# Optimization experiments

Measured on AMD Instinct MI355X. Metric: run time of the kernel, lower is better.

The kernel has to match this reference:

```python
import jax, jax.numpy as jnp
import numpy as np

N0 = 3190      # len(x_0), hardcoded via `edges[0] += 3190` in the source
N_NEW = 16384  # test batch size
T = 60         # num_features (seq len)
C = 5          # n_diagnosis_codes
H = 20         # emb_size == hidden_size == input_size
HC = 15        # hidden_channels
NCLS = 3
L = 4          # lstm layers
K = 5          # neighbors kept per new node
E0 = 31900     # edges in pickled base graph


def setup_inputs() -> dict:
    key = jax.random.key(0)
    ks = jax.random.split(key, 21)
    s = 0.2  # ~ pytorch uniform(-1/sqrt(20), 1/sqrt(20)) scale, avoids LSTM saturation
    return {
        "x": jax.random.uniform(ks[0], (T, N_NEW, C), jnp.float32),
        "x_0": jax.random.normal(ks[1], (N0, H), jnp.float32),
        "emb_w": jax.random.normal(ks[2], (C, H), jnp.float32) * s,
        "lstm_Wih": jax.random.normal(ks[3], (L, 4 * H, H), jnp.float32) * s,
        "lstm_Whh": jax.random.normal(ks[4], (L, 4 * H, H), jnp.float32) * s,
        "lstm_bih": jax.random.normal(ks[5], (L, 4 * H), jnp.float32) * s,
        "lstm_bhh": jax.random.normal(ks[6], (L, 4 * H), jnp.float32) * s,
        "attn_w1": jax.random.normal(ks[7], (64, H), jnp.float32) * s,
        "attn_b1": jax.random.normal(ks[8], (64,), jnp.float32) * s,
        "attn_w2": jax.random.normal(ks[9], (1, 64), jnp.float32) * s,
        "attn_b2": jax.random.normal(ks[10], (1,), jnp.float32) * s,
        "w1l": jax.random.normal(ks[11], (HC, H), jnp.float32) * s,
        "w1r": jax.random.normal(ks[12], (HC, H), jnp.float32) * s,
        "b1": jax.random.normal(ks[13], (HC,), jnp.float32) * s,
        "w2l": jax.random.normal(ks[14], (H, HC), jnp.float32) * s,
        "w2r": jax.random.normal(ks[15], (H, HC), jnp.float32) * s,
        "b2": jax.random.normal(ks[16], (H,), jnp.float32) * s,
        "wlin": jax.random.normal(ks[17], (NCLS, H), jnp.float32) * s,
        "blin": jax.random.normal(ks[18], (NCLS,), jnp.float32) * s,
        "edge_0": jax.random.randint(ks[19], (2, E0), 0, N0, dtype=jnp.int32),
    }


def _lstm_layer(inp, Wih, Whh, bih, bhh):
    # inp: [T, B, D]; PyTorch gate order i, f, g, o
    B = inp.shape[1]
    Hh = Whh.shape[1]
    b = bih + bhh

    def step(carry, xt):
        h, c = carry
        g = xt @ Wih.T + h @ Whh.T + b  # [B, 4H]
        i, f, gg, o = jnp.split(g, 4, axis=-1)
        c = jax.nn.sigmoid(f) * c + jax.nn.sigmoid(i) * jnp.tanh(gg)
        h = jax.nn.sigmoid(o) * jnp.tanh(c)
        return (h, c), h

    init = (jnp.zeros((B, Hh), inp.dtype), jnp.zeros((B, Hh), inp.dtype))
    _, hs = jax.lax.scan(step, init, inp)
    return hs  # [T, B, H]


def _sage(xn, src, dst, Wl, Wr, b, num_nodes):
    # PyG SAGEConv (mean aggr): lin_l(mean_{j in N(i)} x_j) + lin_r(x_i); bias in lin_l
    msg = xn[src]  # gather  [E, D]
    s = jax.ops.segment_sum(msg, dst, num_segments=num_nodes)
    cnt = jax.ops.segment_sum(jnp.ones(dst.shape, xn.dtype), dst, num_segments=num_nodes)
    mean = s / jnp.maximum(cnt, 1.0)[:, None]
    return mean @ Wl.T + xn @ Wr.T + b


def _forward(x, x_0, emb_w, lstm_Wih, lstm_Whh, lstm_bih, lstm_bhh,
             attn_w1, attn_b1, attn_w2, attn_b2,
             w1l, w1r, b1, w2l, w2r, b2, wlin, blin, edge_0):
    # (x[...,None] * emb_w).sum over codes == weighted embedding mix, then relu
    h = jax.nn.relu(jnp.einsum('tnc,ce->tne', x, emb_w))  # [T, N_new, H]
    for l in range(L):
        h = _lstm_layer(h, lstm_Wih[l], lstm_Whh[l], lstm_bih[l], lstm_bhh[l])
    enc = jnp.transpose(h, (1, 0, 2))  # [N_new, T, H]
    # SelfAttention: Linear(H,64) -> ReLU -> Linear(64,1) -> softmax over time
    hid = jax.nn.relu(jnp.einsum('nth,kh->ntk', enc, attn_w1) + attn_b1)
    energy = jnp.einsum('ntk,ok->nto', hid, attn_w2) + attn_b2  # [N_new, T, 1]
    w = jax.nn.softmax(energy[..., 0], axis=1)
    xh = jnp.sum(enc * w[..., None], axis=1)  # [N_new, H]
    # cosine similarity against the fixed base nodes (memory-bound [N_new, N0] matrix)
    a = (xh @ x_0.T) / jnp.linalg.norm(xh, axis=1, keepdims=True) / jnp.linalg.norm(x_0, axis=1)[None, :]
    top6_v, top6_i = jax.lax.top_k(a, 6)
    # per-row branch: drop self-match (sim == 1.0) else drop 6th neighbor
    exact = top6_v[:, 0] == 1.0
    top5 = jnp.where(exact[:, None], top6_i[:, 1:], top6_i[:, :K])  # [N_new, 5]
    # torch.where(A>0) enumerates row-major with sorted cols; rows have exactly 5 ones
    src = jnp.sort(top5, axis=1).reshape(-1)  # base-node endpoints
    dst = jnp.repeat(jnp.arange(N_NEW, dtype=src.dtype), K) + N0  # new-node endpoints (offset)
    edges_new = jnp.stack([src, dst])  # direction base -> new (after the swap in source)
    edges_all = jnp.concatenate([edge_0.astype(src.dtype), edges_new], axis=1)
    xcat = jnp.concatenate([x_0, xh], axis=0)  # [N0 + N_new, H]
    num_nodes = N0 + N_NEW
    o = jax.nn.relu(_sage(xcat, edge_0[0], edge_0[1], w1l, w1r, b1, num_nodes))
    # F.dropout with training=False is identity (test-time module)
    o = _sage(o, edges_all[0], edges_all[1], w2l, w2r, b2, num_nodes)
    o = jax.nn.softmax(o @ wlin.T + blin, axis=1)
    return o[N0:]


def reference(x, x_0, emb_w, lstm_Wih, lstm_Whh, lstm_bih, lstm_bhh,
              attn_w1, attn_b1, attn_w2, attn_b2,
              w1l, w1r, b1, w2l, w2r, b2, wlin, blin, edge_0):
    return _forward(x, x_0, emb_w, lstm_Wih, lstm_Whh, lstm_bih, lstm_bhh,
                    attn_w1, attn_b1, attn_w2, attn_b2,
                    w1l, w1r, b1, w2l, w2r, b2, wlin, blin, edge_0)
```

## Files before the change

kernel.cpp:

```cpp
#include <hip/hip_runtime.h>
#include <math.h>

#define T_ 60
#define N_ 16384
#define C_ 5
#define H_ 20
#define G_ 80
#define HC_ 15
#define N0_ 3190
#define E0_ 31900
#define K_ 5

#define OFF_SEQ   0
#define OFF_XH    (T_*N_*H_)
#define OFF_XHN   (OFF_XH + N_*H_)
#define OFF_NX0   (OFF_XHN + N_)
#define OFF_RX0   (OFF_NX0 + N0_)
#define OFF_TOP5  (OFF_RX0 + N0_)
#define OFF_SUM1  (OFF_TOP5 + N_*K_)
#define OFF_CNT1  (OFF_SUM1 + N0_*H_)
#define OFF_OBASE (OFF_CNT1 + N0_)

__device__ __forceinline__ float sigf(float x) {
  return __fdividef(1.0f, 1.0f + __expf(-x));
}
__device__ __forceinline__ float tanhf_fast(float x) {
  float xc = fminf(fmaxf(x, -44.0f), 44.0f);
  float e = __expf(2.0f * xc);
  return __fdividef(e - 1.0f, e + 1.0f);
}


#define LWV 160

template <bool FIRST>
__global__ void __launch_bounds__(256, 2) lstm_wpe_kernel(
    const float* __restrict__ xg,
    const float* __restrict__ embw,
    const float* __restrict__ Wih,
    const float* __restrict__ Whh,
    const float* __restrict__ bih,
    const float* __restrict__ bhh,
    float* __restrict__ seq) {
  __shared__ __align__(16) float wst[3200];
  __shared__ __align__(16) float wsh[4 * LWV];
  const int tid = threadIdx.x;

  for (int i = tid; i < 3200; i += 256) {
    int r = i / 40, col = i % 40;
    wst[i] = (col < 20) ? Wih[r * 20 + col] : Whh[r * 20 + (col - 20)];
  }
  __syncthreads();

  const int lane = tid & 63;
  const int w = tid >> 6;
  const int rg = lane >> 2;
  const int cg = lane & 3;
  const int n = (blockIdx.x << 2) + w;
  float* zb  = &wsh[w * LWV];
  float* gr  = &wsh[w * LWV + 64];
  float* raw = &wsh[w * LWV + 144];

  float wr[5][10];
  {
    const float* bp = &wst[(rg * 5) * 40 + cg * 10];
#pragma unroll
    for (int j = 0; j < 5; j++)
#pragma unroll
      for (int m = 0; m < 10; m++) wr[j][m] = bp[j * 40 + m];
  }
#pragma unroll
  for (int j = 0; j < 5; j++)
#pragma unroll
    for (int m = 0; m < 10; m++) asm volatile("" : "+v"(wr[j][m]));

  const bool isU = (lane < 20);
  const int u = isU ? lane : 0;
  const float bi = bih[u] + bhh[u];
  const float bf = bih[20 + u] + bhh[20 + u];
  const float bg = bih[40 + u] + bhh[40 + u];
  const float bo = bih[60 + u] + bhh[60 + u];
  float e0 = 0, e1 = 0, e2 = 0, e3 = 0, e4 = 0;
  if (FIRST) {
    e0 = embw[u]; e1 = embw[20 + u]; e2 = embw[40 + u];
    e3 = embw[60 + u]; e4 = embw[80 + u];
  }

  if (isU) {
    int col = 20 + u;
    zb[(col / 10) * 12 + (col % 10)] = 0.0f;
  }
  if (FIRST) {
    if (lane < 5) raw[lane] = xg[(size_t)n * 5 + lane];
    asm volatile("s_waitcnt lgkmcnt(0)" ::: "memory");
    if (isU) {
      float a = raw[0] * e0 + raw[1] * e1 + raw[2] * e2 + raw[3] * e3 + raw[4] * e4;
      zb[(u / 10) * 12 + (u % 10)] = fmaxf(a, 0.0f);
    }
  } else {
    if (isU) zb[(u / 10) * 12 + (u % 10)] = seq[(size_t)n * 20 + u];
  }
  asm volatile("s_waitcnt lgkmcnt(0)" ::: "memory");

  float c = 0.0f;
  for (int t = 0; t < T_; t++) {
    float px = 0.0f;
    if (t + 1 < T_) {
      if (FIRST) {
        if (lane < 5) px = xg[(size_t)(t + 1) * (N_ * 5) + n * 5 + lane];
      } else {
        if (isU) px = seq[(size_t)(t + 1) * (N_ * 20) + n * 20 + u];
      }
    }
    float z[10];
    {
      const float* zp = zb + cg * 12;
      float4 a4 = *reinterpret_cast<const float4*>(zp);
      float4 b4 = *reinterpret_cast<const float4*>(zp + 4);
      float2 c2 = *reinterpret_cast<const float2*>(zp + 8);
      z[0] = a4.x; z[1] = a4.y; z[2] = a4.z; z[3] = a4.w;
      z[4] = b4.x; z[5] = b4.y; z[6] = b4.z; z[7] = b4.w;
      z[8] = c2.x; z[9] = c2.y;
    }
    float acc[5];
#pragma unroll
    for (int j = 0; j < 5; j++) {
      float a = wr[j][0] * z[0];
#pragma unroll
      for (int m = 1; m < 10; m++) a += wr[j][m] * z[m];
      acc[j] = a;
    }
#pragma unroll
    for (int j = 0; j < 5; j++) acc[j] += __shfl_xor(acc[j], 1, 64);
#pragma unroll
    for (int j = 0; j < 5; j++) acc[j] += __shfl_xor(acc[j], 2, 64);
    if (cg == 0) {
#pragma unroll
      for (int j = 0; j < 5; j++) gr[rg * 5 + j] = acc[j];
    }
    asm volatile("s_waitcnt lgkmcnt(0)" ::: "memory");
    if (isU) {
      float gi = gr[u] + bi;
      float gf = gr[20 + u] + bf;
      float gg = gr[40 + u] + bg;
      float go = gr[60 + u] + bo;
      float cu = sigf(gf) * c + sigf(gi) * tanhf_fast(gg);
      c = cu;
      float h = sigf(go) * tanhf_fast(cu);
      seq[(size_t)t * (N_ * 20) + n * 20 + u] = h;
      int col = 20 + u;
      zb[(col / 10) * 12 + (col % 10)] = h;
    }
    if (t + 1 < T_) {
      if (FIRST) {
        if (lane < 5) raw[lane] = px;
        asm volatile("s_waitcnt lgkmcnt(0) vmcnt(0)" ::: "memory");
        if (isU) {
          float a = raw[0] * e0 + raw[1] * e1 + raw[2] * e2 + raw[3] * e3 + raw[4] * e4;
          zb[(u / 10) * 12 + (u % 10)] = fmaxf(a, 0.0f);
        }
      } else {
        if (isU) zb[(u / 10) * 12 + (u % 10)] = px;
      }
    }
    asm volatile("s_waitcnt lgkmcnt(0)" ::: "memory");
  }
}

__global__ void __launch_bounds__(256) attn_kernel(
    const float* __restrict__ seq, const float* __restrict__ w1,
    const float* __restrict__ b1v, const float* __restrict__ w2,
    const float* __restrict__ b2v, float* __restrict__ xh, float* __restrict__ xhn) {
  const int wv = threadIdx.x >> 6;
  const int t = threadIdx.x & 63;
  const int n = (blockIdx.x << 2) + wv;
  const bool act = (t < T_);
  float enc[20];
#pragma unroll
  for (int k = 0; k < 20; k++) enc[k] = 0.0f;
  if (act) {
    const float* p = seq + (t * N_ + n) * H_;
#pragma unroll
    for (int q = 0; q < 5; q++) {
      float4 v = *reinterpret_cast<const float4*>(p + 4 * q);
      enc[4 * q] = v.x; enc[4 * q + 1] = v.y; enc[4 * q + 2] = v.z; enc[4 * q + 3] = v.w;
    }
  }
  float e = -3.0e38f;
  if (act) {
    e = b2v[0];
#pragma unroll 4
    for (int k = 0; k < 64; k++) {
      float s = b1v[k];
      const float* wr = w1 + k * 20;
#pragma unroll
      for (int m = 0; m < 20; m++) s += wr[m] * enc[m];
      s = fmaxf(s, 0.0f);
      e += w2[k] * s;
    }
  }
  float mx = e;
#pragma unroll
  for (int d = 32; d; d >>= 1) mx = fmaxf(mx, __shfl_xor(mx, d, 64));
  float p_ = act ? __expf(e - mx) : 0.0f;
  float sm = p_;
#pragma unroll
  for (int d = 32; d; d >>= 1) sm += __shfl_xor(sm, d, 64);
  float w = __fdividef(p_, sm);
  float a[20];
#pragma unroll
  for (int k = 0; k < 20; k++) a[k] = enc[k] * w;
#pragma unroll
  for (int d = 1; d < 64; d <<= 1) {
#pragma unroll
    for (int k = 0; k < 20; k++) a[k] += __shfl_xor(a[k], d, 64);
  }
  if (t == 0) {
    float* op = xh + n * 20;
    float s2 = 0.0f;
#pragma unroll
    for (int k = 0; k < 20; k++) s2 += a[k] * a[k];
#pragma unroll
    for (int q = 0; q < 5; q++) {
      float4 v; v.x = a[4 * q]; v.y = a[4 * q + 1]; v.z = a[4 * q + 2]; v.w = a[4 * q + 3];
      *reinterpret_cast<float4*>(op + 4 * q) = v;
    }
    xhn[n] = sqrtf(s2);
  }
}

__global__ void __launch_bounds__(256) x0norm_kernel(const float* __restrict__ x0,
                                                     float* __restrict__ nx0,
                                                     float* __restrict__ rx0) {
  int j = blockIdx.x * 256 + threadIdx.x;
  if (j >= N0_) return;
  float s = 0.f;
#pragma unroll
  for (int k = 0; k < 20; k++) { float v = x0[j * 20 + k]; s += v * v; }
  float nv = sqrtf(s);
  nx0[j] = nv;
  rx0[j] = 1.0f / nv;
}

__device__ __forceinline__ bool better_(float v1, int i1, float v2, int i2) {
  return (v1 > v2) || (v1 == v2 && i1 < i2);
}

__device__ __forceinline__ void merge6(float tv[6], int ti[6], int d) {
  float cv[12]; int ci[12];
#pragma unroll
  for (int z = 0; z < 6; z++) { cv[z] = tv[z]; ci[z] = ti[z]; }
#pragma unroll
  for (int z = 0; z < 6; z++) {
    cv[6 + z] = __shfl_xor(tv[z], d, 64);
    ci[6 + z] = __shfl_xor(ti[z], d, 64);
  }
#pragma unroll
  for (int o = 0; o < 6; o++) {
    float bv = -3.0e38f; int bi = 0x7fffffff; int bm = -1;
#pragma unroll
    for (int m = 0; m < 12; m++) {
      bool bt = better_(cv[m], ci[m], bv, bi);
      if (bt) { bv = cv[m]; bi = ci[m]; bm = m; }
    }
    tv[o] = bv; ti[o] = bi;
#pragma unroll
    for (int m = 0; m < 12; m++) if (m == bm) cv[m] = -3.0e38f;
  }
}

__global__ void __launch_bounds__(256) topk_kernel(
    const float* __restrict__ x0, const float* __restrict__ xh,
    const float* __restrict__ xhn, const float* __restrict__ nx0,
    const float* __restrict__ rx0, int* __restrict__ top5) {
  const int gt = blockIdx.x * 256 + threadIdx.x;
  const int i = gt >> 4, sub = gt & 15;
  float q[20];
  const float* qp = xh + i * 20;
#pragma unroll
  for (int z = 0; z < 5; z++) {
    float4 v = *reinterpret_cast<const float4*>(qp + 4 * z);
    q[4 * z] = v.x; q[4 * z + 1] = v.y; q[4 * z + 2] = v.z; q[4 * z + 3] = v.w;
  }
  float tv[6]; int ti[6];
#pragma unroll
  for (int z = 0; z < 6; z++) { tv[z] = -1.0e30f; ti[z] = 0x7fffffff; }
  for (int j = sub; j < N0_; j += 16) {
    const float* xr = x0 + j * 20;
    float d0 = 0.f;
#pragma unroll
    for (int k = 0; k < 20; k++) d0 += q[k] * xr[k];
    float key = d0 * rx0[j];
    if (key > tv[5]) {
      tv[5] = key; ti[5] = j;
#pragma unroll
      for (int z = 5; z >= 1; z--) {
        bool sw = better_(tv[z], ti[z], tv[z - 1], ti[z - 1]);
        if (sw) {
          float fv = tv[z]; tv[z] = tv[z - 1]; tv[z - 1] = fv;
          int iv = ti[z]; ti[z] = ti[z - 1]; ti[z - 1] = iv;
        }
      }
    }
  }
  merge6(tv, ti, 1);
  merge6(tv, ti, 2);
  merge6(tv, ti, 4);
  merge6(tv, ti, 8);
  if (sub == 0) {
    const float* xr = x0 + ti[0] * 20;
    float d0 = 0.f;
#pragma unroll
    for (int k = 0; k < 20; k++) d0 += q[k] * xr[k];
    float a = (d0 / xhn[i]) / nx0[ti[0]];
    int base = (a == 1.0f) ? 1 : 0;
#pragma unroll
    for (int z = 0; z < 5; z++) top5[i * 5 + z] = ti[base + z];
  }
}

__global__ void __launch_bounds__(256) scatter_kernel(const int* __restrict__ edge,
                                                      const float* __restrict__ x0,
                                                      float* sum1, float* cnt1) {
  int e = blockIdx.x * 256 + threadIdx.x;
  if (e >= E0_) return;
  int s = edge[e], d = edge[E0_ + e];
  const float* xr = x0 + s * 20;
  float* dr = sum1 + d * 20;
#pragma unroll
  for (int k = 0; k < 20; k++) atomicAdd(dr + k, xr[k]);
  atomicAdd(cnt1 + d, 1.0f);
}

__global__ void __launch_bounds__(256) base_kernel(
    const float* __restrict__ x0, const float* __restrict__ sum1,
    const float* __restrict__ cnt1, const float* __restrict__ w1l,
    const float* __restrict__ w1r, const float* __restrict__ b1,
    float* __restrict__ obase) {
  int j = blockIdx.x * 256 + threadIdx.x;
  if (j >= N0_) return;
  float cm = fmaxf(cnt1[j], 1.0f);
  float mean[20], xv[20];
#pragma unroll
  for (int k = 0; k < 20; k++) {
    mean[k] = sum1[j * 20 + k] / cm;
    xv[k] = x0[j * 20 + k];
  }
#pragma unroll
  for (int c = 0; c < HC_; c++) {
    float a = b1[c];
#pragma unroll
    for (int k = 0; k < 20; k++) a += mean[k] * w1l[c * 20 + k];
#pragma unroll
    for (int k = 0; k < 20; k++) a += xv[k] * w1r[c * 20 + k];
    obase[j * HC_ + c] = fmaxf(a, 0.0f);
  }
}

__global__ void __launch_bounds__(256) final_kernel(
    const float* __restrict__ xh, const int* __restrict__ top5,
    const float* __restrict__ obase, const float* __restrict__ w1r,
    const float* __restrict__ b1, const float* __restrict__ w2l,
    const float* __restrict__ w2r, const float* __restrict__ b2,
    const float* __restrict__ wlin, const float* __restrict__ blin,
    float* __restrict__ out) {
  int n = blockIdx.x * 256 + threadIdx.x;
  if (n >= N_) return;
  float xq[20];
#pragma unroll
  for (int k = 0; k < 20; k++) xq[k] = xh[n * 20 + k];
  float onw[15];
#pragma unroll
  for (int c = 0; c < HC_; c++) {
    float a = b1[c];
#pragma unroll
    for (int k = 0; k < 20; k++) a += xq[k] * w1r[c * 20 + k];
    onw[c] = fmaxf(a, 0.0f);
  }
  float mean[15];
#pragma unroll
  for (int c = 0; c < HC_; c++) mean[c] = 0.0f;
#pragma unroll
  for (int z = 0; z < K_; z++) {
    int idx = top5[n * 5 + z];
#pragma unroll
    for (int c = 0; c < HC_; c++) mean[c] += obase[idx * HC_ + c];
  }
#pragma unroll
  for (int c = 0; c < HC_; c++) mean[c] = mean[c] / 5.0f;
  float lg[3];
#pragma unroll
  for (int cl = 0; cl < 3; cl++) lg[cl] = blin[cl];
#pragma unroll
  for (int dd = 0; dd < 20; dd++) {
    float v = b2[dd];
#pragma unroll
    for (int c = 0; c < HC_; c++) v += mean[c] * w2l[dd * HC_ + c] + onw[c] * w2r[dd * HC_ + c];
#pragma unroll
    for (int cl = 0; cl < 3; cl++) lg[cl] += v * wlin[cl * 20 + dd];
  }
  float m = fmaxf(lg[0], fmaxf(lg[1], lg[2]));
  float e0 = expf(lg[0] - m), e1 = expf(lg[1] - m), e2 = expf(lg[2] - m);
  float s = e0 + e1 + e2;
  out[n * 3 + 0] = e0 / s;
  out[n * 3 + 1] = e1 / s;
  out[n * 3 + 2] = e2 / s;
}

extern "C" void kernel_launch(void* const* d_in, const int* in_sizes, int n_in,
                              void* d_out, int out_size, void* d_ws, size_t ws_size,
                              hipStream_t stream) {
  const float* x    = (const float*)d_in[0];
  const float* x0   = (const float*)d_in[1];
  const float* embw = (const float*)d_in[2];
  const float* Wih  = (const float*)d_in[3];
  const float* Whh  = (const float*)d_in[4];
  const float* bih  = (const float*)d_in[5];
  const float* bhh  = (const float*)d_in[6];
  const float* aw1  = (const float*)d_in[7];
  const float* ab1  = (const float*)d_in[8];
  const float* aw2  = (const float*)d_in[9];
  const float* ab2  = (const float*)d_in[10];
  const float* w1l  = (const float*)d_in[11];
  const float* w1r  = (const float*)d_in[12];
  const float* b1   = (const float*)d_in[13];
  const float* w2l  = (const float*)d_in[14];
  const float* w2r  = (const float*)d_in[15];
  const float* b2   = (const float*)d_in[16];
  const float* wlin = (const float*)d_in[17];
  const float* blin = (const float*)d_in[18];
  const int* edge0  = (const int*)d_in[19];

  float* ws    = (float*)d_ws;
  float* seq   = ws + OFF_SEQ;
  float* xh    = ws + OFF_XH;
  float* xhn   = ws + OFF_XHN;
  float* nx0   = ws + OFF_NX0;
  float* rx0   = ws + OFF_RX0;
  int*   top5  = (int*)(ws + OFF_TOP5);
  float* sum1  = ws + OFF_SUM1;
  float* cnt1  = ws + OFF_CNT1;
  float* obase = ws + OFF_OBASE;
  float* out   = (float*)d_out;

  hipMemsetAsync(sum1, 0, (size_t)(N0_ * H_ + N0_) * sizeof(float), stream);
  lstm_wpe_kernel<true><<<N_ / 4, 256, 0, stream>>>(x, embw, Wih, Whh, bih, bhh, seq);
  for (int l = 1; l < 4; l++)
    lstm_wpe_kernel<false><<<N_ / 4, 256, 0, stream>>>(x, embw, Wih + l * 1600,
                                                       Whh + l * 1600, bih + l * 80,
                                                       bhh + l * 80, seq);
  attn_kernel<<<N_ / 4, 256, 0, stream>>>(seq, aw1, ab1, aw2, ab2, xh, xhn);
  x0norm_kernel<<<(N0_ + 255) / 256, 256, 0, stream>>>(x0, nx0, rx0);
  topk_kernel<<<(N_ * 16) / 256, 256, 0, stream>>>(x0, xh, xhn, nx0, rx0, top5);
  scatter_kernel<<<(E0_ + 255) / 256, 256, 0, stream>>>(edge0, x0, sum1, cnt1);
  base_kernel<<<(N0_ + 255) / 256, 256, 0, stream>>>(x0, sum1, cnt1, w1l, w1r, b1, obase);
  final_kernel<<<N_ / 256, 256, 0, stream>>>(xh, top5, obase, w1r, b1, w2l, w2r, b2,
                                             wlin, blin, out);
}
```

Before: 1.340 ms.

## Process two sequences per wavefront in LSTM kernel to reuse register weights

Each wavefront in the LSTM layer kernel now advances two batch elements instead of one. The 50 register-resident weights are reused for two dot products per step, halving the number of wavefronts and blocks. This amortises the serial latency of each step (shuffles, LDS round trips, waits) across two sequences and raises ILP. In exchange it uses more registers and LDS, which may lower occupancy, and there are half as many waves to hide latency.

```diff
diff --git a/kernel.cpp b/kernel.cpp
--- a/kernel.cpp
+++ b/kernel.cpp
@@ -31,10 +31,10 @@
 }
 
 
-#define LWV 160
+#define LWV 272
 
 template <bool FIRST>
-__global__ void __launch_bounds__(256, 2) lstm_wpe_kernel(
+__global__ void __launch_bounds__(256, 2) lstm_wpe2_kernel(
     const float* __restrict__ xg,
     const float* __restrict__ embw,
     const float* __restrict__ Wih,
@@ -56,10 +56,13 @@
   const int w = tid >> 6;
   const int rg = lane >> 2;
   const int cg = lane & 3;
-  const int n = (blockIdx.x << 2) + w;
-  float* zb  = &wsh[w * LWV];
-  float* gr  = &wsh[w * LWV + 64];
-  float* raw = &wsh[w * LWV + 144];
+  const int n0 = (blockIdx.x << 3) + (w << 1);
+  const int n1 = n0 + 1;
+  float* zb0 = &wsh[w * LWV];
+  float* zb1 = zb0 + 48;
+  float* gr0 = zb0 + 96;
+  float* gr1 = zb0 + 176;
+  float* raw = zb0 + 256;
 
   float wr[5][10];
   {
@@ -74,8 +77,15 @@
 #pragma unroll
     for (int m = 0; m < 10; m++) asm volatile("" : "+v"(wr[j][m]));
 
-  const bool isU = (lane < 20);
-  const int u = isU ? lane : 0;
+  const bool isU0 = (lane < 20);
+  const bool isU1 = (lane >= 32 && lane < 52);
+  const bool isU = isU0 || isU1;
+  const int u = isU0 ? lane : (isU1 ? (lane - 32) : 0);
+  const int myn = isU1 ? n1 : n0;
+  float* myzb = isU1 ? zb1 : zb0;
+  const float* mygr = isU1 ? gr1 : gr0;
+  const float* myraw = isU1 ? (raw + 5) : raw;
+
   const float bi = bih[u] + bhh[u];
   const float bf = bih[20 + u] + bhh[20 + u];
   const float bg = bih[40 + u] + bhh[40 + u];
@@ -88,17 +98,19 @@
 
   if (isU) {
     int col = 20 + u;
-    zb[(col / 10) * 12 + (col % 10)] = 0.0f;
+    myzb[(col / 10) * 12 + (col % 10)] = 0.0f;
   }
   if (FIRST) {
-    if (lane < 5) raw[lane] = xg[(size_t)n * 5 + lane];
+    if (lane < 5) raw[lane] = xg[(size_t)n0 * 5 + lane];
+    if (lane >= 32 && lane < 37) raw[5 + (lane - 32)] = xg[(size_t)n1 * 5 + (lane - 32)];
     asm volatile("s_waitcnt lgkmcnt(0)" ::: "memory");
     if (isU) {
-      float a = raw[0] * e0 + raw[1] * e1 + raw[2] * e2 + raw[3] * e3 + raw[4] * e4;
-      zb[(u / 10) * 12 + (u % 10)] = fmaxf(a, 0.0f);
+      float a = myraw[0] * e0 + myraw[1] * e1 + myraw[2] * e2 + myraw[3] * e3
+              + myraw[4] * e4;
+      myzb[(u / 10) * 12 + (u % 10)] = fmaxf(a, 0.0f);
     }
   } else {
-    if (isU) zb[(u / 10) * 12 + (u % 10)] = seq[(size_t)n * 20 + u];
+    if (isU) myzb[(u / 10) * 12 + (u % 10)] = seq[(size_t)myn * 20 + u];
   }
   asm volatile("s_waitcnt lgkmcnt(0)" ::: "memory");
 
@@ -107,60 +119,78 @@
     float px = 0.0f;
     if (t + 1 < T_) {
       if (FIRST) {
-        if (lane < 5) px = xg[(size_t)(t + 1) * (N_ * 5) + n * 5 + lane];
+        if (lane < 5) px = xg[(size_t)(t + 1) * (N_ * 5) + n0 * 5 + lane];
+        if (lane >= 32 && lane < 37)
+          px = xg[(size_t)(t + 1) * (N_ * 5) + n1 * 5 + (lane - 32)];
       } else {
-        if (isU) px = seq[(size_t)(t + 1) * (N_ * 20) + n * 20 + u];
+        if (isU) px = seq[(size_t)(t + 1) * (N_ * 20) + myn * 20 + u];
       }
     }
-    float z[10];
+    float z0[10], z1[10];
     {
-      const float* zp = zb + cg * 12;
+      const float* zp = zb0 + cg * 12;
       float4 a4 = *reinterpret_cast<const float4*>(zp);
       float4 b4 = *reinterpret_cast<const float4*>(zp + 4);
       float2 c2 = *reinterpret_cast<const float2*>(zp + 8);
-      z[0] = a4.x; z[1] = a4.y; z[2] = a4.z; z[3] = a4.w;
-      z[4] = b4.x; z[5] = b4.y; z[6] = b4.z; z[7] = b4.w;
-      z[8] = c2.x; z[9] = c2.y;
-    }
-    float acc[5];
+      z0[0] = a4.x; z0[1] = a4.y; z0[2] = a4.z; z0[3] = a4.w;
+      z0[4] = b4.x; z0[5] = b4.y; z0[6] = b4.z; z0[7] = b4.w;
+      z0[8] = c2.x; z0[9] = c2.y;
+      const float* zq = zb1 + cg * 12;
+      float4 d4 = *reinterpret_cast<const float4*>(zq);
+      float4 e4_ = *reinterpret_cast<const float4*>(zq + 4);
+      float2 f2 = *reinterpret_cast<const float2*>(zq + 8);
+      z1[0] = d4.x; z1[1] = d4.y; z1[2] = d4.z; z1[3] = d4.w;
+      z1[4] = e4_.x; z1[5] = e4_.y; z1[6] = e4_.z; z1[7] = e4_.w;
+      z1[8] = f2.x; z1[9] = f2.y;
+    }
+    float acc0[5], acc1[5];
 #pragma unroll
     for (int j = 0; j < 5; j++) {
-      float a = wr[j][0] * z[0];
-#pragma unroll
-      for (int m = 1; m < 10; m++) a += wr[j][m] * z[m];
-      acc[j] = a;
-    }
-#pragma unroll
-    for (int j = 0; j < 5; j++) acc[j] += __shfl_xor(acc[j], 1, 64);
-#pragma unroll
-    for (int j = 0; j < 5; j++) acc[j] += __shfl_xor(acc[j], 2, 64);
+      float a0 = wr[j][0] * z0[0];
+      float a1 = wr[j][0] * z1[0];
+#pragma unroll
+      for (int m = 1; m < 10; m++) {
+        a0 += wr[j][m] * z0[m];
+        a1 += wr[j][m] * z1[m];
+      }
+      acc0[j] = a0; acc1[j] = a1;
+    }
+#pragma unroll
+    for (int j = 0; j < 5; j++) { acc0[j] += __shfl_xor(acc0[j], 1, 64);
+                                  acc1[j] += __shfl_xor(acc1[j], 1, 64); }
+#pragma unroll
+    for (int j = 0; j < 5; j++) { acc0[j] += __shfl_xor(acc0[j], 2, 64);
+                                  acc1[j] += __shfl_xor(acc1[j], 2, 64); }
     if (cg == 0) {
 #pragma unroll
-      for (int j = 0; j < 5; j++) gr[rg * 5 + j] = acc[j];
+      for (int j = 0; j < 5; j++) { gr0[rg * 5 + j] = acc0[j];
+                                    gr1[rg * 5 + j] = acc1[j]; }
     }
     asm volatile("s_waitcnt lgkmcnt(0)" ::: "memory");
     if (isU) {
-      float gi = gr[u] + bi;
-      float gf = gr[20 + u] + bf;
-      float gg = gr[40 + u] + bg;
-      float go = gr[60 + u] + bo;
+      float gi = mygr[u] + bi;
+      float gf = mygr[20 + u] + bf;
+      float gg = mygr[40 + u] + bg;
+      float go = mygr[60 + u] + bo;
       float cu = sigf(gf) * c + sigf(gi) * tanhf_fast(gg);
       c = cu;
       float h = sigf(go) * tanhf_fast(cu);
-      seq[(size_t)t * (N_ * 20) + n * 20 + u] = h;
+      seq[(size_t)t * (N_ * 20) + myn * 20 + u] = h;
       int col = 20 + u;
-      zb[(col / 10) * 12 + (col % 10)] = h;
+      myzb[(col / 10) * 12 + (col % 10)] = h;
     }
     if (t + 1 < T_) {
       if (FIRST) {
         if (lane < 5) raw[lane] = px;
+        if (lane >= 32 && lane < 37) raw[5 + (lane - 32)] = px;
         asm volatile("s_waitcnt lgkmcnt(0) vmcnt(0)" ::: "memory");
         if (isU) {
-          float a = raw[0] * e0 + raw[1] * e1 + raw[2] * e2 + raw[3] * e3 + raw[4] * e4;
-          zb[(u / 10) * 12 + (u % 10)] = fmaxf(a, 0.0f);
+          float a = myraw[0] * e0 + myraw[1] * e1 + myraw[2] * e2 + myraw[3] * e3
+                  + myraw[4] * e4;
+          myzb[(u / 10) * 12 + (u % 10)] = fmaxf(a, 0.0f);
         }
       } else {
-        if (isU) zb[(u / 10) * 12 + (u % 10)] = px;
+        if (isU) myzb[(u / 10) * 12 + (u % 10)] = px;
       }
     }
     asm volatile("s_waitcnt lgkmcnt(0)" ::: "memory");
@@ -444,11 +474,11 @@
   float* out   = (float*)d_out;
 
   hipMemsetAsync(sum1, 0, (size_t)(N0_ * H_ + N0_) * sizeof(float), stream);
-  lstm_wpe_kernel<true><<<N_ / 4, 256, 0, stream>>>(x, embw, Wih, Whh, bih, bhh, seq);
+  lstm_wpe2_kernel<true><<<N_ / 8, 256, 0, stream>>>(x, embw, Wih, Whh, bih, bhh, seq);
   for (int l = 1; l < 4; l++)
-    lstm_wpe_kernel<false><<<N_ / 4, 256, 0, stream>>>(x, embw, Wih + l * 1600,
-                                                       Whh + l * 1600, bih + l * 80,
-                                                       bhh + l * 80, seq);
+    lstm_wpe2_kernel<false><<<N_ / 8, 256, 0, stream>>>(x, embw, Wih + l * 1600,
+                                                        Whh + l * 1600, bih + l * 80,
+                                                        bhh + l * 80, seq);
   attn_kernel<<<N_ / 4, 256, 0, stream>>>(seq, aw1, ab1, aw2, ab2, xh, xhn);
   x0norm_kernel<<<(N0_ + 255) / 256, 256, 0, stream>>>(x0, nx0, rx0);
   topk_kernel<<<(N_ * 16) / 256, 256, 0, stream>>>(x0, xh, xhn, nx0, rx0, top5);
```

After: 1.123 ms. 16.2% less time.

## Process four sequences per wavefront in LSTM kernel to amortize register weights

Applied to the files above, without the earlier changes.

Each wavefront now handles four batch elements instead of one, reusing its register-resident weight slice for four matvecs per timestep and having all 64 lanes (two halves) do the gate nonlinearities. The shared-memory weight staging and block sync are removed; weights load straight from global memory. This aims to cut the per-step latency and instruction overhead that one sequence per wave left underused. In exchange, grid size drops fourfold (1024 blocks), which lowers parallelism, and register pressure rises.

```diff
diff --git a/kernel.cpp b/kernel.cpp
--- a/kernel.cpp
+++ b/kernel.cpp
@@ -31,10 +31,10 @@
 }
 
 
-#define LWV 160
+#define LWV 544
 
 template <bool FIRST>
-__global__ void __launch_bounds__(256, 2) lstm_wpe_kernel(
+__global__ void __launch_bounds__(256, 2) lstm_wpe4_kernel(
     const float* __restrict__ xg,
     const float* __restrict__ embw,
     const float* __restrict__ Wih,
@@ -42,125 +42,202 @@
     const float* __restrict__ bih,
     const float* __restrict__ bhh,
     float* __restrict__ seq) {
-  __shared__ __align__(16) float wst[3200];
   __shared__ __align__(16) float wsh[4 * LWV];
   const int tid = threadIdx.x;
-
-  for (int i = tid; i < 3200; i += 256) {
-    int r = i / 40, col = i % 40;
-    wst[i] = (col < 20) ? Wih[r * 20 + col] : Whh[r * 20 + (col - 20)];
-  }
-  __syncthreads();
-
   const int lane = tid & 63;
   const int w = tid >> 6;
   const int rg = lane >> 2;
   const int cg = lane & 3;
-  const int n = (blockIdx.x << 2) + w;
+  const int n0 = (blockIdx.x << 4) + (w << 2);
   float* zb  = &wsh[w * LWV];
-  float* gr  = &wsh[w * LWV + 64];
-  float* raw = &wsh[w * LWV + 144];
+  float* gr  = zb + 192;
+  float* raw = zb + 512;
 
   float wr[5][10];
   {
-    const float* bp = &wst[(rg * 5) * 40 + cg * 10];
+    const float* wbase = (cg < 2) ? (Wih + (rg * 5) * 20 + cg * 10)
+                                  : (Whh + (rg * 5) * 20 + (cg - 2) * 10);
 #pragma unroll
     for (int j = 0; j < 5; j++)
 #pragma unroll
-      for (int m = 0; m < 10; m++) wr[j][m] = bp[j * 40 + m];
+      for (int m = 0; m < 10; m++) wr[j][m] = wbase[j * 20 + m];
   }
 #pragma unroll
   for (int j = 0; j < 5; j++)
 #pragma unroll
     for (int m = 0; m < 10; m++) asm volatile("" : "+v"(wr[j][m]));
 
-  const bool isU = (lane < 20);
-  const int u = isU ? lane : 0;
-  const float bi = bih[u] + bhh[u];
-  const float bf = bih[20 + u] + bhh[20 + u];
-  const float bg = bih[40 + u] + bhh[40 + u];
-  const float bo = bih[60 + u] + bhh[60 + u];
+  const bool isUh = (lane & 31) < 20;
+  const int ub = lane & 31;
+  const int elA = (lane >= 32) ? 1 : 0;
+  const int elB = elA + 2;
+  float* zbA = zb + elA * 48;
+  float* zbB = zb + elB * 48;
+  const float* grA_ = gr + elA * 80;
+  const float* grB_ = gr + elB * 80;
+  const float* rawA = raw + elA * 5;
+  const float* rawB = raw + elB * 5;
+  const int xslot = (ub / 10) * 12 + (ub % 10);
+  const int hslot = (2 + ub / 10) * 12 + (ub % 10);
+
+  const float bi = bih[ub] + bhh[ub];
+  const float bf = bih[20 + ub] + bhh[20 + ub];
+  const float bg = bih[40 + ub] + bhh[40 + ub];
+  const float bo = bih[60 + ub] + bhh[60 + ub];
   float e0 = 0, e1 = 0, e2 = 0, e3 = 0, e4 = 0;
   if (FIRST) {
-    e0 = embw[u]; e1 = embw[20 + u]; e2 = embw[40 + u];
-    e3 = embw[60 + u]; e4 = embw[80 + u];
-  }
-
-  if (isU) {
-    int col = 20 + u;
-    zb[(col / 10) * 12 + (col % 10)] = 0.0f;
-  }
+    e0 = embw[ub]; e1 = embw[20 + ub]; e2 = embw[40 + ub];
+    e3 = embw[60 + ub]; e4 = embw[80 + ub];
+  }
+
+  if (isUh) { zbA[hslot] = 0.0f; zbB[hslot] = 0.0f; }
   if (FIRST) {
-    if (lane < 5) raw[lane] = xg[(size_t)n * 5 + lane];
+    if (lane < 20) raw[lane] = xg[(size_t)n0 * 5 + lane];
     asm volatile("s_waitcnt lgkmcnt(0)" ::: "memory");
-    if (isU) {
-      float a = raw[0] * e0 + raw[1] * e1 + raw[2] * e2 + raw[3] * e3 + raw[4] * e4;
-      zb[(u / 10) * 12 + (u % 10)] = fmaxf(a, 0.0f);
+    if (isUh) {
+      float a = rawA[0] * e0 + rawA[1] * e1 + rawA[2] * e2 + rawA[3] * e3
+              + rawA[4] * e4;
+      zbA[xslot] = fmaxf(a, 0.0f);
+      float b = rawB[0] * e0 + rawB[1] * e1 + rawB[2] * e2 + rawB[3] * e3
+              + rawB[4] * e4;
+      zbB[xslot] = fmaxf(b, 0.0f);
     }
   } else {
-    if (isU) zb[(u / 10) * 12 + (u % 10)] = seq[(size_t)n * 20 + u];
+    if (isUh) {
+      zbA[xslot] = seq[(size_t)(n0 + elA) * 20 + ub];
+      zbB[xslot] = seq[(size_t)(n0 + elB) * 20 + ub];
+    }
   }
   asm volatile("s_waitcnt lgkmcnt(0)" ::: "memory");
 
-  float c = 0.0f;
+  float cA = 0.0f, cB = 0.0f;
   for (int t = 0; t < T_; t++) {
-    float px = 0.0f;
+    float pxA = 0.0f, pxB = 0.0f;
     if (t + 1 < T_) {
       if (FIRST) {
-        if (lane < 5) px = xg[(size_t)(t + 1) * (N_ * 5) + n * 5 + lane];
+        if (lane < 20) pxA = xg[(size_t)(t + 1) * (N_ * 5) + n0 * 5 + lane];
       } else {
-        if (isU) px = seq[(size_t)(t + 1) * (N_ * 20) + n * 20 + u];
-      }
-    }
-    float z[10];
+        if (isUh) {
+          const float* sp = seq + (size_t)(t + 1) * (N_ * 20) + n0 * 20;
+          pxA = sp[elA * 20 + ub];
+          pxB = sp[elB * 20 + ub];
+        }
+      }
+    }
+    float acc0[5], acc1[5], acc2[5], acc3[5];
     {
-      const float* zp = zb + cg * 12;
+      const float* zp = zb + 0 * 48 + cg * 12;
       float4 a4 = *reinterpret_cast<const float4*>(zp);
       float4 b4 = *reinterpret_cast<const float4*>(zp + 4);
       float2 c2 = *reinterpret_cast<const float2*>(zp + 8);
-      z[0] = a4.x; z[1] = a4.y; z[2] = a4.z; z[3] = a4.w;
-      z[4] = b4.x; z[5] = b4.y; z[6] = b4.z; z[7] = b4.w;
-      z[8] = c2.x; z[9] = c2.y;
-    }
-    float acc[5];
+      float z[10] = {a4.x, a4.y, a4.z, a4.w, b4.x, b4.y, b4.z, b4.w, c2.x, c2.y};
+#pragma unroll
+      for (int j = 0; j < 5; j++) {
+        float a = wr[j][0] * z[0];
+#pragma unroll
+        for (int m = 1; m < 10; m++) a += wr[j][m] * z[m];
+        acc0[j] = a;
+      }
+    }
+    {
+      const float* zp = zb + 1 * 48 + cg * 12;
+      float4 a4 = *reinterpret_cast<const float4*>(zp);
+      float4 b4 = *reinterpret_cast<const float4*>(zp + 4);
+      float2 c2 = *reinterpret_cast<const float2*>(zp + 8);
+      float z[10] = {a4.x, a4.y, a4.z, a4.w, b4.x, b4.y, b4.z, b4.w, c2.x, c2.y};
+#pragma unroll
+      for (int j = 0; j < 5; j++) {
+        float a = wr[j][0] * z[0];
+#pragma unroll
+        for (int m = 1; m < 10; m++) a += wr[j][m] * z[m];
+        acc1[j] = a;
+      }
+    }
+    {
+      const float* zp = zb + 2 * 48 + cg * 12;
+      float4 a4 = *reinterpret_cast<const float4*>(zp);
+      float4 b4 = *reinterpret_cast<const float4*>(zp + 4);
+      float2 c2 = *reinterpret_cast<const float2*>(zp + 8);
+      float z[10] = {a4.x, a4.y, a4.z, a4.w, b4.x, b4.y, b4.z, b4.w, c2.x, c2.y};
+#pragma unroll
+      for (int j = 0; j < 5; j++) {
+        float a = wr[j][0] * z[0];
+#pragma unroll
+        for (int m = 1; m < 10; m++) a += wr[j][m] * z[m];
+        acc2[j] = a;
+      }
+    }
+    {
+      const float* zp = zb + 3 * 48 + cg * 12;
+      float4 a4 = *reinterpret_cast<const float4*>(zp);
+      float4 b4 = *reinterpret_cast<const float4*>(zp + 4);
+      float2 c2 = *reinterpret_cast<const float2*>(zp + 8);
+      float z[10] = {a4.x, a4.y, a4.z, a4.w, b4.x, b4.y, b4.z, b4.w, c2.x, c2.y};
+#pragma unroll
+      for (int j = 0; j < 5; j++) {
+        float a = wr[j][0] * z[0];
+#pragma unroll
+        for (int m = 1; m < 10; m++) a += wr[j][m] * z[m];
+        acc3[j] = a;
+      }
+    }
 #pragma unroll
     for (int j = 0; j < 5; j++) {
-      float a = wr[j][0] * z[0];
-#pragma unroll
-      for (int m = 1; m < 10; m++) a += wr[j][m] * z[m];
-      acc[j] = a;
-    }
-#pragma unroll
-    for (int j = 0; j < 5; j++) acc[j] += __shfl_xor(acc[j], 1, 64);
-#pragma unroll
-    for (int j = 0; j < 5; j++) acc[j] += __shfl_xor(acc[j], 2, 64);
-    if (cg == 0) {
-#pragma unroll
-      for (int j = 0; j < 5; j++) gr[rg * 5 + j] = acc[j];
+      acc0[j] += __shfl_xor(acc0[j], 1, 64);
+      acc1[j] += __shfl_xor(acc1[j], 1, 64);
+      acc2[j] += __shfl_xor(acc2[j], 1, 64);
+      acc3[j] += __shfl_xor(acc3[j], 1, 64);
+    }
+#pragma unroll
+    for (int j = 0; j < 5; j++) {
+      acc0[j] += __shfl_xor(acc0[j], 2, 64);
+      acc1[j] += __shfl_xor(acc1[j], 2, 64);
+      acc2[j] += __shfl_xor(acc2[j], 2, 64);
+      acc3[j] += __shfl_xor(acc3[j], 2, 64);
+    }
+#pragma unroll
+    for (int j = 0; j < 5; j++) {
+      float s = acc0[j];
+      if (cg == 1) s = acc1[j];
+      if (cg == 2) s = acc2[j];
+      if (cg == 3) s = acc3[j];
+      gr[cg * 80 + rg * 5 + j] = s;
     }
     asm volatile("s_waitcnt lgkmcnt(0)" ::: "memory");
-    if (isU) {
-      float gi = gr[u] + bi;
-      float gf = gr[20 + u] + bf;
-      float gg = gr[40 + u] + bg;
-      float go = gr[60 + u] + bo;
-      float cu = sigf(gf) * c + sigf(gi) * tanhf_fast(gg);
-      c = cu;
-      float h = sigf(go) * tanhf_fast(cu);
-      seq[(size_t)t * (N_ * 20) + n * 20 + u] = h;
-      int col = 20 + u;
-      zb[(col / 10) * 12 + (col % 10)] = h;
+    if (isUh) {
+      float giA = grA_[ub] + bi;
+      float gfA = grA_[20 + ub] + bf;
+      float ggA = grA_[40 + ub] + bg;
+      float goA = grA_[60 + ub] + bo;
+      float giB = grB_[ub] + bi;
+      float gfB = grB_[20 + ub] + bf;
+      float ggB = grB_[40 + ub] + bg;
+      float goB = grB_[60 + ub] + bo;
+      float cuA = sigf(gfA) * cA + sigf(giA) * tanhf_fast(ggA);
+      float cuB = sigf(gfB) * cB + sigf(giB) * tanhf_fast(ggB);
+      cA = cuA; cB = cuB;
+      float hA = sigf(goA) * tanhf_fast(cuA);
+      float hB = sigf(goB) * tanhf_fast(cuB);
+      float* op = seq + (size_t)t * (N_ * 20) + n0 * 20;
+      op[elA * 20 + ub] = hA;
+      op[elB * 20 + ub] = hB;
+      zbA[hslot] = hA;
+      zbB[hslot] = hB;
     }
     if (t + 1 < T_) {
       if (FIRST) {
-        if (lane < 5) raw[lane] = px;
+        if (lane < 20) raw[lane] = pxA;
         asm volatile("s_waitcnt lgkmcnt(0) vmcnt(0)" ::: "memory");
-        if (isU) {
-          float a = raw[0] * e0 + raw[1] * e1 + raw[2] * e2 + raw[3] * e3 + raw[4] * e4;
-          zb[(u / 10) * 12 + (u % 10)] = fmaxf(a, 0.0f);
+        if (isUh) {
+          float a = rawA[0] * e0 + rawA[1] * e1 + rawA[2] * e2 + rawA[3] * e3
+                  + rawA[4] * e4;
+          zbA[xslot] = fmaxf(a, 0.0f);
+          float b = rawB[0] * e0 + rawB[1] * e1 + rawB[2] * e2 + rawB[3] * e3
+                  + rawB[4] * e4;
+          zbB[xslot] = fmaxf(b, 0.0f);
         }
       } else {
-        if (isU) zb[(u / 10) * 12 + (u % 10)] = px;
+        if (isUh) { zbA[xslot] = pxA; zbB[xslot] = pxB; }
       }
     }
     asm volatile("s_waitcnt lgkmcnt(0)" ::: "memory");
@@ -444,11 +521,11 @@
   float* out   = (float*)d_out;
 
   hipMemsetAsync(sum1, 0, (size_t)(N0_ * H_ + N0_) * sizeof(float), stream);
-  lstm_wpe_kernel<true><<<N_ / 4, 256, 0, stream>>>(x, embw, Wih, Whh, bih, bhh, seq);
+  lstm_wpe4_kernel<true><<<N_ / 16, 256, 0, stream>>>(x, embw, Wih, Whh, bih, bhh, seq);
   for (int l = 1; l < 4; l++)
-    lstm_wpe_kernel<false><<<N_ / 4, 256, 0, stream>>>(x, embw, Wih + l * 1600,
-                                                       Whh + l * 1600, bih + l * 80,
-                                                       bhh + l * 80, seq);
+    lstm_wpe4_kernel<false><<<N_ / 16, 256, 0, stream>>>(x, embw, Wih + l * 1600,
+                                                         Whh + l * 1600, bih + l * 80,
+                                                         bhh + l * 80, seq);
   attn_kernel<<<N_ / 4, 256, 0, stream>>>(seq, aw1, ab1, aw2, ab2, xh, xhn);
   x0norm_kernel<<<(N0_ + 255) / 256, 256, 0, stream>>>(x0, nx0, rx0);
   topk_kernel<<<(N_ * 16) / 256, 256, 0, stream>>>(x0, xh, xhn, nx0, rx0, top5);
```

Measured after the change: 1.111 ms. -17.1%, faster.
